# Optimization experiments

Measured on AMD Instinct MI355X. Metric: run time of the kernel, lower is better.

The kernel has to match this reference:

```python
import jax, jax.numpy as jnp
import numpy as np

D_MODEL = 1024
NUM_HEADS = 16
BATCH = 2
SEQ = 2048


def setup_inputs() -> dict:
    key = jax.random.key(0)
    ks = jax.random.split(key, 5)
    scale = 1.0 / np.sqrt(D_MODEL)
    x = jax.random.normal(ks[0], (BATCH, SEQ, D_MODEL), dtype=jnp.float32)
    Wq = jax.random.normal(ks[1], (D_MODEL, D_MODEL), dtype=jnp.float32) * scale
    Wk = jax.random.normal(ks[2], (D_MODEL, D_MODEL), dtype=jnp.float32) * scale
    Wv = jax.random.normal(ks[3], (D_MODEL, D_MODEL), dtype=jnp.float32) * scale
    Wo = jax.random.normal(ks[4], (D_MODEL, D_MODEL), dtype=jnp.float32) * scale
    return {"x": x, "Wq": Wq, "Wk": Wk, "Wv": Wv, "Wo": Wo}


def reference(x, Wq, Wk, Wv, Wo):
    b, s, d_model = x.shape
    h = NUM_HEADS
    d_head = d_model // h
    # projections (Linear with weight [out,in]: y = x @ W^T)
    def split_heads(y):
        return y.reshape(b, s, h, d_head).transpose(0, 2, 1, 3)  # b h s d
    q = split_heads(x @ Wq.T)
    k = split_heads(x @ Wk.T)
    v = split_heads(x @ Wv.T)
    # full (non-flash) attention, as in the original
    att = jnp.einsum('bhsd,bhtd->bhst', q, k) / jnp.sqrt(jnp.float32(d_head)).astype(x.dtype)
    att = jax.nn.softmax(att, axis=-1)
    out = jnp.einsum('bhst,bhtd->bhsd', att, v)
    out = out.transpose(0, 2, 1, 3).reshape(b, s, d_model)
    return out @ Wo.T
```

## Files before the change

kernel.cpp:

```cpp
#include <hip/hip_runtime.h>
#include <stdint.h>

typedef __bf16 bf16_t;
typedef __bf16 bf16x4 __attribute__((ext_vector_type(4)));
typedef __bf16 bf16x8 __attribute__((ext_vector_type(8)));
typedef float  f32x4  __attribute__((ext_vector_type(4)));
typedef float  f32x16 __attribute__((ext_vector_type(16)));

#define D_MODEL 1024
#define SEQ     2048
#define BATCH   2
#define NHEAD   16
#define DHEAD   64
#define NROWS   (BATCH*SEQ)
#define LDT     72
#define LDP     72

__device__ __forceinline__ void async_ld16(const bf16_t* g, bf16_t* l) {
    __builtin_amdgcn_global_load_lds(
        (const __attribute__((address_space(1))) uint32_t*)(uintptr_t)g,
        (__attribute__((address_space(3))) uint32_t*)(uintptr_t)l,
        16, 0, 0);
}

__device__ __forceinline__ bf16x8 cvt8(f32x4 lo, f32x4 hi) {
    bf16x8 o;
#pragma unroll
    for (int i = 0; i < 4; ++i) { o[i] = (bf16_t)lo[i]; o[4 + i] = (bf16_t)hi[i]; }
    return o;
}

__global__ void __launch_bounds__(256)
k_cvt(const float* __restrict__ w0, const float* __restrict__ w1,
      const float* __restrict__ w2, const float* __restrict__ w3,
      const float* __restrict__ x,
      bf16_t* __restrict__ o0, bf16_t* __restrict__ o1,
      bf16_t* __restrict__ o2, bf16_t* __restrict__ o3,
      bf16_t* __restrict__ ox)
{
    const int blk = blockIdx.x;
    const float* s; bf16_t* d; int bi;
    if (blk < 2048) { s = x; d = ox; bi = blk; }
    else {
        const int t = blk - 2048, sel = t >> 9; bi = t & 511;
        s = (sel == 0) ? w0 : (sel == 1) ? w1 : (sel == 2) ? w2 : w3;
        d = (sel == 0) ? o0 : (sel == 1) ? o1 : (sel == 2) ? o2 : o3;
    }
    const size_t i = ((size_t)bi * 256 + threadIdx.x) * 8;
    *(bf16x8*)(d + i) = cvt8(*(const f32x4*)(s + i), *(const f32x4*)(s + i + 4));
}

template <int OUT_MODE>
__device__ __forceinline__ void gemm128(bf16_t* __restrict__ smem,
                                        const bf16_t* __restrict__ X,
                                        const bf16_t* __restrict__ W,
                                        void* __restrict__ Yv,
                                        int m0, int n0, float oscale)
{
    bf16_t* lA = smem;
    bf16_t* lB = smem + 128 * 32;

    const int tid  = threadIdx.x;
    const int lane = tid & 63;
    const int w    = tid >> 6;
    const int l15  = lane & 15;
    const int quad = lane >> 4;

    const int c0 = tid, c1 = tid + 256;
    const int r0 = c0 >> 2, r1 = c1 >> 2;
    const int kc0 = (c0 & 3) ^ ((r0 >> 1) & 3);
    const int kc1 = (c1 & 3) ^ ((r1 >> 1) & 3);
    const bf16_t* gA0 = X + (size_t)(m0 + r0) * D_MODEL + kc0 * 8;
    const bf16_t* gA1 = X + (size_t)(m0 + r1) * D_MODEL + kc1 * 8;
    const bf16_t* gB0 = W + (size_t)(n0 + r0) * D_MODEL + kc0 * 8;
    const bf16_t* gB1 = W + (size_t)(n0 + r1) * D_MODEL + kc1 * 8;

    int am[4], bn[4];
    const int mw = (w >> 1) * 64, nw = (w & 1) * 64;
#pragma unroll
    for (int i = 0; i < 4; ++i) {
        const int ra = mw + i * 16 + l15;
        am[i] = ra * 32 + (quad ^ ((ra >> 1) & 3)) * 8;
        const int rb = nw + i * 16 + l15;
        bn[i] = rb * 32 + (quad ^ ((rb >> 1) & 3)) * 8;
    }

    f32x4 acc[4][4];
#pragma unroll
    for (int i = 0; i < 4; ++i)
#pragma unroll
        for (int j = 0; j < 4; ++j) acc[i][j] = f32x4{0.f, 0.f, 0.f, 0.f};

    for (int k0 = 0; k0 < D_MODEL; k0 += 32) {
        __syncthreads();
        async_ld16(gA0 + k0, &lA[c0 * 8]);
        async_ld16(gA1 + k0, &lA[c1 * 8]);
        async_ld16(gB0 + k0, &lB[c0 * 8]);
        async_ld16(gB1 + k0, &lB[c1 * 8]);
        __syncthreads();

        bf16x8 af[4], bfr[4];
#pragma unroll
        for (int i = 0; i < 4; ++i) af[i]  = *(const bf16x8*)&lA[am[i]];
#pragma unroll
        for (int i = 0; i < 4; ++i) bfr[i] = *(const bf16x8*)&lB[bn[i]];
#pragma unroll
        for (int mi = 0; mi < 4; ++mi)
#pragma unroll
            for (int ni = 0; ni < 4; ++ni)
                acc[mi][ni] = __builtin_amdgcn_mfma_f32_16x16x32_bf16(
                    af[mi], bfr[ni], acc[mi][ni], 0, 0, 0);
    }

    if constexpr (OUT_MODE == 1) {
        bf16_t* lT = smem;
#pragma unroll
        for (int h0 = 0; h0 < 2; ++h0) {
            __syncthreads();
            if ((w >> 1) == h0) {
#pragma unroll
                for (int mi = 0; mi < 4; ++mi)
#pragma unroll
                    for (int ni = 0; ni < 4; ++ni) {
                        bf16x4 pk;
#pragma unroll
                        for (int r = 0; r < 4; ++r)
                            pk[r] = (bf16_t)(acc[mi][ni][r] * oscale);
                        const int col = nw + ni * 16 + l15;
                        *(bf16x4*)&lT[col * LDT + mi * 16 + quad * 4] = pk;
                    }
            }
            __syncthreads();
            const int col = tid & 127;
            const int seg = tid >> 7;
            const int brow = m0 + h0 * 64;
            const int b = brow >> 11, sb = brow & 2047;
            const int cg = n0 + col;
            bf16_t* dst = (bf16_t*)Yv +
                ((size_t)((b << 4) | (cg >> 6)) * 64 + (cg & 63)) * SEQ + sb;
#pragma unroll
            for (int u = 0; u < 4; ++u)
                *(bf16x8*)(dst + seg * 32 + u * 8) =
                    *(const bf16x8*)&lT[col * LDT + seg * 32 + u * 8];
        }
    } else {
#pragma unroll
        for (int mi = 0; mi < 4; ++mi)
#pragma unroll
            for (int ni = 0; ni < 4; ++ni)
#pragma unroll
                for (int r = 0; r < 4; ++r) {
                    const int row = m0 + mw + mi * 16 + quad * 4 + r;
                    const int col = n0 + nw + ni * 16 + l15;
                    const float vv = acc[mi][ni][r] * oscale;
                    if constexpr (OUT_MODE == 0)
                        ((bf16_t*)Yv)[(size_t)row * D_MODEL + col] = (bf16_t)vv;
                    else
                        ((float*)Yv)[(size_t)row * D_MODEL + col] = vv;
                }
    }
}

__global__ void __launch_bounds__(256, 3)
k_gemm_qkv(const bf16_t* __restrict__ X,
           const bf16_t* __restrict__ Wq, const bf16_t* __restrict__ Wk,
           const bf16_t* __restrict__ Wv,
           bf16_t* __restrict__ Qb, bf16_t* __restrict__ Kb, bf16_t* __restrict__ Vt)
{
    __shared__ __align__(16) bf16_t smem[128 * LDT];
    const int sel = blockIdx.y >> 3;
    const int n0  = (blockIdx.y & 7) * 128;
    const int m0  = blockIdx.x * 128;
    if (sel == 0)      gemm128<0>(smem, X, Wq, Qb, m0, n0, 0.125f);
    else if (sel == 1) gemm128<0>(smem, X, Wk, Kb, m0, n0, 1.0f);
    else               gemm128<1>(smem, X, Wv, Vt, m0, n0, 1.0f);
}

__global__ void __launch_bounds__(256, 3)
k_gemm_out(const bf16_t* __restrict__ X, const bf16_t* __restrict__ W,
           float* __restrict__ Y)
{
    __shared__ __align__(16) bf16_t smem[128 * LDT];
    gemm128<2>(smem, X, W, Y, blockIdx.x * 128, blockIdx.y * 128, 1.0f);
}

__global__ void __launch_bounds__(256, 4)
k_attn(const bf16_t* __restrict__ Qb, const bf16_t* __restrict__ Kb,
       const bf16_t* __restrict__ Vt, bf16_t* __restrict__ Ob)
{
    __shared__ __align__(16) bf16_t lK[64 * 64];
    __shared__ __align__(16) bf16_t lV[64 * 64];
    __shared__ __align__(16) bf16_t Pm[64 * LDP];
    __shared__ float sbuf[2][64];

    const int tid  = threadIdx.x;
    const int lane = tid & 63;
    const int w    = tid >> 6;
    const int l31  = lane & 31;
    const int h    = lane >> 5;
    const int a    = w & 1;
    const int b    = w >> 1;

    const int bh = blockIdx.x;
    const int b_ = bh >> 4, hh = bh & 15;
    const int q0 = blockIdx.y * 64;

    const size_t base = (size_t)b_ * SEQ * D_MODEL + (size_t)hh * DHEAD;
    const bf16_t* Qp = Qb + base;
    const bf16_t* Kp = Kb + base;
    const bf16_t* Vp = Vt + (size_t)bh * DHEAD * SEQ;

    const int qrow = q0 + b * 32 + l31;
    bf16x8 qf[4];
#pragma unroll
    for (int c = 0; c < 4; ++c)
        qf[c] = *(const bf16x8*)&Qp[(size_t)qrow * D_MODEL + c * 16 + h * 8];

    const int c0 = tid, c1 = tid + 256;
    const int r0 = c0 >> 3, g0 = (c0 & 7) ^ (r0 & 7);
    const int r1 = c1 >> 3, g1 = (c1 & 7) ^ (r1 & 7);
    const bf16_t* gK0 = Kp + (size_t)r0 * D_MODEL + g0 * 8;
    const bf16_t* gK1 = Kp + (size_t)r1 * D_MODEL + g1 * 8;
    const bf16_t* gV0 = Vp + (size_t)r0 * SEQ + g0 * 8;
    const bf16_t* gV1 = Vp + (size_t)r1 * SEQ + g1 * 8;

    const int frow = a * 32 + l31;
    int koff[4], poff[4];
#pragma unroll
    for (int c = 0; c < 4; ++c) {
        const int ci = 2 * c + h;
        koff[c] = frow * 64 + (ci ^ (frow & 7)) * 8;
        poff[c] = (b * 32 + l31) * LDP + c * 16 + h * 8;
    }

    f32x16 acc_o;
#pragma unroll
    for (int i = 0; i < 16; ++i) acc_o[i] = 0.f;
    float rsum = 0.f;

    for (int kv0 = 0; kv0 < SEQ; kv0 += 64) {
        __syncthreads();
        async_ld16(gK0 + (size_t)kv0 * D_MODEL, &lK[c0 * 8]);
        async_ld16(gK1 + (size_t)kv0 * D_MODEL, &lK[c1 * 8]);
        async_ld16(gV0 + kv0, &lV[c0 * 8]);
        async_ld16(gV1 + kv0, &lV[c1 * 8]);
        __syncthreads();

        f32x16 st;
#pragma unroll
        for (int i = 0; i < 16; ++i) st[i] = 0.f;
#pragma unroll
        for (int c = 0; c < 4; ++c) {
            bf16x8 kf = *(const bf16x8*)&lK[koff[c]];
            st = __builtin_amdgcn_mfma_f32_32x32x16_bf16(kf, qf[c], st, 0, 0, 0);
        }

#pragma unroll
        for (int g = 0; g < 4; ++g) {
            bf16x4 pp;
#pragma unroll
            for (int r = 0; r < 4; ++r) {
                const float e = __expf(st[g * 4 + r]);
                pp[r] = (bf16_t)e;
                rsum += e;
            }
            *(bf16x4*)&Pm[(b * 32 + l31) * LDP + a * 32 + g * 8 + h * 4] = pp;
        }
        __syncthreads();

#pragma unroll
        for (int c = 0; c < 4; ++c) {
            bf16x8 pf = *(const bf16x8*)&Pm[poff[c]];
            bf16x8 vf = *(const bf16x8*)&lV[koff[c]];
            acc_o = __builtin_amdgcn_mfma_f32_32x32x16_bf16(pf, vf, acc_o, 0, 0, 0);
        }
    }

    rsum += __shfl_xor(rsum, 32);
    if (lane < 32) sbuf[a][b * 32 + l31] = rsum;
    __syncthreads();

#pragma unroll
    for (int g = 0; g < 4; ++g)
#pragma unroll
        for (int r = 0; r < 4; ++r) {
            const int ql  = r + 8 * g + 4 * h;
            const float lsum = sbuf[0][b * 32 + ql] + sbuf[1][b * 32 + ql];
            const int row = b_ * SEQ + q0 + b * 32 + ql;
            const int col = hh * DHEAD + a * 32 + l31;
            Ob[(size_t)row * D_MODEL + col] = (bf16_t)(acc_o[g * 4 + r] / lsum);
        }
}

extern "C" void kernel_launch(void* const* d_in, const int* in_sizes, int n_in,
                              void* d_out, int out_size, void* d_ws, size_t ws_size,
                              hipStream_t stream)
{
    const float* x  = (const float*)d_in[0];
    const float* Wq = (const float*)d_in[1];
    const float* Wk = (const float*)d_in[2];
    const float* Wv = (const float*)d_in[3];
    const float* Wo = (const float*)d_in[4];
    float* out = (float*)d_out;

    const size_t wmat = (size_t)D_MODEL * D_MODEL;
    const size_t mat  = (size_t)NROWS * D_MODEL;
    bf16_t* Wqb = (bf16_t*)d_ws;
    bf16_t* Wkb = Wqb + wmat;
    bf16_t* Wvb = Wkb + wmat;
    bf16_t* Wob = Wvb + wmat;
    bf16_t* Xb  = Wob + wmat;
    bf16_t* Qb  = Xb + mat;
    bf16_t* Kb  = Qb + mat;
    bf16_t* Vt  = Kb + mat;
    bf16_t* Ab  = Qb;

    dim3 blk(256);
    k_cvt<<<dim3(4096), blk, 0, stream>>>(Wq, Wk, Wv, Wo, x, Wqb, Wkb, Wvb, Wob, Xb);
    k_gemm_qkv<<<dim3(32, 24), blk, 0, stream>>>(Xb, Wqb, Wkb, Wvb, Qb, Kb, Vt);
    k_attn<<<dim3(32, 32), blk, 0, stream>>>(Qb, Kb, Vt, Ab);
    k_gemm_out<<<dim3(32, 8), blk, 0, stream>>>(Ab, Wob, out);
}
```

Measured before the change: 187.6 us.

## Keep attention P in registers via lane shuffles; give each wave 32 query rows

The attention kernel now has each wave own 32 full query rows and compute scores for all 64 keys itself, instead of splitting the key dimension across wave pairs. The exp'd probabilities are rearranged into MFMA A-operand layout with cross-half-wave shuffles rather than written to and read back from shared memory. This drops the P buffer and one barrier per KV tile, and doubles the query block to 128 rows so each K/V tile load is reused by twice as many queries. In exchange it uses more registers per thread (two accumulators), so launch bounds drop to 2 blocks per CU, and the grid is halved.

```diff
diff --git a/kernel.cpp b/kernel.cpp
--- a/kernel.cpp
+++ b/kernel.cpp
@@ -14,7 +14,6 @@
 #define DHEAD   64
 #define NROWS   (BATCH*SEQ)
 #define LDT     72
-#define LDP     72
 
 __device__ __forceinline__ void async_ld16(const bf16_t* g, bf16_t* l) {
     __builtin_amdgcn_global_load_lds(
@@ -28,6 +27,13 @@
 #pragma unroll
     for (int i = 0; i < 4; ++i) { o[i] = (bf16_t)lo[i]; o[4 + i] = (bf16_t)hi[i]; }
     return o;
+}
+
+__device__ __forceinline__ bf16x4 shflx32(bf16x4 v) {
+    union { bf16x4 b; long long u; } x;
+    x.b = v;
+    x.u = __shfl_xor(x.u, 32);
+    return x.b;
 }
 
 __global__ void __launch_bounds__(256)
@@ -184,33 +190,30 @@
     gemm128<2>(smem, X, W, Y, blockIdx.x * 128, blockIdx.y * 128, 1.0f);
 }
 
-__global__ void __launch_bounds__(256, 4)
+__global__ void __launch_bounds__(256, 2)
 k_attn(const bf16_t* __restrict__ Qb, const bf16_t* __restrict__ Kb,
        const bf16_t* __restrict__ Vt, bf16_t* __restrict__ Ob)
 {
     __shared__ __align__(16) bf16_t lK[64 * 64];
     __shared__ __align__(16) bf16_t lV[64 * 64];
-    __shared__ __align__(16) bf16_t Pm[64 * LDP];
-    __shared__ float sbuf[2][64];
+    __shared__ float sbuf[128];
 
     const int tid  = threadIdx.x;
     const int lane = tid & 63;
     const int w    = tid >> 6;
     const int l31  = lane & 31;
     const int h    = lane >> 5;
-    const int a    = w & 1;
-    const int b    = w >> 1;
 
     const int bh = blockIdx.x;
     const int b_ = bh >> 4, hh = bh & 15;
-    const int q0 = blockIdx.y * 64;
+    const int q0 = blockIdx.y * 128;
 
     const size_t base = (size_t)b_ * SEQ * D_MODEL + (size_t)hh * DHEAD;
     const bf16_t* Qp = Qb + base;
     const bf16_t* Kp = Kb + base;
     const bf16_t* Vp = Vt + (size_t)bh * DHEAD * SEQ;
 
-    const int qrow = q0 + b * 32 + l31;
+    const int qrow = q0 + w * 32 + l31;
     bf16x8 qf[4];
 #pragma unroll
     for (int c = 0; c < 4; ++c)
@@ -218,24 +221,27 @@
 
     const int c0 = tid, c1 = tid + 256;
     const int r0 = c0 >> 3, g0 = (c0 & 7) ^ (r0 & 7);
-    const int r1 = c1 >> 3, g1 = (c1 & 7) ^ (r1 & 7);
+    const int r1 = r0 + 32;
     const bf16_t* gK0 = Kp + (size_t)r0 * D_MODEL + g0 * 8;
-    const bf16_t* gK1 = Kp + (size_t)r1 * D_MODEL + g1 * 8;
+    const bf16_t* gK1 = Kp + (size_t)r1 * D_MODEL + g0 * 8;
     const bf16_t* gV0 = Vp + (size_t)r0 * SEQ + g0 * 8;
-    const bf16_t* gV1 = Vp + (size_t)r1 * SEQ + g1 * 8;
-
-    const int frow = a * 32 + l31;
-    int koff[4], poff[4];
-#pragma unroll
-    for (int c = 0; c < 4; ++c) {
-        const int ci = 2 * c + h;
-        koff[c] = frow * 64 + (ci ^ (frow & 7)) * 8;
-        poff[c] = (b * 32 + l31) * LDP + c * 16 + h * 8;
-    }
-
-    f32x16 acc_o;
-#pragma unroll
-    for (int i = 0; i < 16; ++i) acc_o[i] = 0.f;
+    const bf16_t* gV1 = Vp + (size_t)r1 * SEQ + g0 * 8;
+
+    int koff[2][4], voff[2][4];
+#pragma unroll
+    for (int half = 0; half < 2; ++half)
+#pragma unroll
+        for (int c = 0; c < 4; ++c) {
+            const int row = half * 32 + l31;
+            koff[half][c] = row * 64 + ((2 * c + h) ^ (row & 7)) * 8;
+            voff[half][c] = koff[half][c];
+        }
+
+    f32x16 acc_o[2];
+#pragma unroll
+    for (int a = 0; a < 2; ++a)
+#pragma unroll
+        for (int i = 0; i < 16; ++i) acc_o[a][i] = 0.f;
     float rsum = 0.f;
 
     for (int kv0 = 0; kv0 < SEQ; kv0 += 64) {
@@ -246,50 +252,69 @@
         async_ld16(gV1 + kv0, &lV[c1 * 8]);
         __syncthreads();
 
-        f32x16 st;
-#pragma unroll
-        for (int i = 0; i < 16; ++i) st[i] = 0.f;
+        bf16x4 pk[2][4];
+#pragma unroll
+        for (int half = 0; half < 2; ++half) {
+            f32x16 st;
+#pragma unroll
+            for (int i = 0; i < 16; ++i) st[i] = 0.f;
+#pragma unroll
+            for (int c = 0; c < 4; ++c) {
+                bf16x8 kf = *(const bf16x8*)&lK[koff[half][c]];
+                st = __builtin_amdgcn_mfma_f32_32x32x16_bf16(kf, qf[c], st, 0, 0, 0);
+            }
+#pragma unroll
+            for (int g = 0; g < 4; ++g)
+#pragma unroll
+                for (int r = 0; r < 4; ++r) {
+                    const float e = __expf(st[g * 4 + r]);
+                    rsum += e;
+                    pk[half][g][r] = (bf16_t)e;
+                }
+        }
+
+        bf16x4 pt[2][4];
+#pragma unroll
+        for (int half = 0; half < 2; ++half)
+#pragma unroll
+            for (int g = 0; g < 4; ++g) pt[half][g] = shflx32(pk[half][g]);
+
+        bf16x8 pf[4];
 #pragma unroll
         for (int c = 0; c < 4; ++c) {
-            bf16x8 kf = *(const bf16x8*)&lK[koff[c]];
-            st = __builtin_amdgcn_mfma_f32_32x32x16_bf16(kf, qf[c], st, 0, 0, 0);
+            const int half = c >> 1, e = 2 * (c & 1);
+            bf16x4 lo = h ? pt[half][e + 1] : pk[half][e];
+            bf16x4 hi = h ? pk[half][e + 1] : pt[half][e];
+#pragma unroll
+            for (int i = 0; i < 4; ++i) { pf[c][i] = lo[i]; pf[c][4 + i] = hi[i]; }
         }
 
 #pragma unroll
-        for (int g = 0; g < 4; ++g) {
-            bf16x4 pp;
+        for (int a = 0; a < 2; ++a)
+#pragma unroll
+            for (int c = 0; c < 4; ++c) {
+                bf16x8 vf = *(const bf16x8*)&lV[voff[a][c]];
+                acc_o[a] = __builtin_amdgcn_mfma_f32_32x32x16_bf16(
+                    pf[c], vf, acc_o[a], 0, 0, 0);
+            }
+    }
+
+    rsum += __shfl_xor(rsum, 32);
+    if (h == 0) sbuf[w * 32 + l31] = rsum;
+    __syncthreads();
+
+#pragma unroll
+    for (int a = 0; a < 2; ++a)
+#pragma unroll
+        for (int g = 0; g < 4; ++g)
 #pragma unroll
             for (int r = 0; r < 4; ++r) {
-                const float e = __expf(st[g * 4 + r]);
-                pp[r] = (bf16_t)e;
-                rsum += e;
+                const int ql  = w * 32 + r + 8 * g + 4 * h;
+                const int row = b_ * SEQ + q0 + ql;
+                const int col = hh * DHEAD + a * 32 + l31;
+                Ob[(size_t)row * D_MODEL + col] =
+                    (bf16_t)(acc_o[a][g * 4 + r] / sbuf[ql]);
             }
-            *(bf16x4*)&Pm[(b * 32 + l31) * LDP + a * 32 + g * 8 + h * 4] = pp;
-        }
-        __syncthreads();
-
-#pragma unroll
-        for (int c = 0; c < 4; ++c) {
-            bf16x8 pf = *(const bf16x8*)&Pm[poff[c]];
-            bf16x8 vf = *(const bf16x8*)&lV[koff[c]];
-            acc_o = __builtin_amdgcn_mfma_f32_32x32x16_bf16(pf, vf, acc_o, 0, 0, 0);
-        }
-    }
-
-    rsum += __shfl_xor(rsum, 32);
-    if (lane < 32) sbuf[a][b * 32 + l31] = rsum;
-    __syncthreads();
-
-#pragma unroll
-    for (int g = 0; g < 4; ++g)
-#pragma unroll
-        for (int r = 0; r < 4; ++r) {
-            const int ql  = r + 8 * g + 4 * h;
-            const float lsum = sbuf[0][b * 32 + ql] + sbuf[1][b * 32 + ql];
-            const int row = b_ * SEQ + q0 + b * 32 + ql;
-            const int col = hh * DHEAD + a * 32 + l31;
-            Ob[(size_t)row * D_MODEL + col] = (bf16_t)(acc_o[g * 4 + r] / lsum);
-        }
 }
 
 extern "C" void kernel_launch(void* const* d_in, const int* in_sizes, int n_in,
@@ -318,6 +343,6 @@
     dim3 blk(256);
     k_cvt<<<dim3(4096), blk, 0, stream>>>(Wq, Wk, Wv, Wo, x, Wqb, Wkb, Wvb, Wob, Xb);
     k_gemm_qkv<<<dim3(32, 24), blk, 0, stream>>>(Xb, Wqb, Wkb, Wvb, Qb, Kb, Vt);
-    k_attn<<<dim3(32, 32), blk, 0, stream>>>(Qb, Kb, Vt, Ab);
+    k_attn<<<dim3(32, 16), blk, 0, stream>>>(Qb, Kb, Vt, Ab);
     k_gemm_out<<<dim3(32, 8), blk, 0, stream>>>(Ab, Wob, out);
 }
```

Result: faster. 182.0 us (-2.9%).
